# Kernel optimization log

Hardware: AMD Instinct MI355X
Metric: run time of the kernel (lower is better)

Reference implementation:

```python
import jax, jax.numpy as jnp
import numpy as np

WIDTH = 768
HEAD = 64

def setup_inputs() -> dict:
    key = jax.random.key(0)
    ks = jax.random.split(key, 8)
    x = jax.random.normal(ks[0], (8, 2048, WIDTH), dtype=jnp.float32)
    mask = jax.random.randint(ks[1], (2048, 2048), 0, 2, dtype=jnp.int32)
    s = 1.0 / np.sqrt(WIDTH)
    Wq = jax.random.normal(ks[2], (WIDTH, HEAD), dtype=jnp.float32) * s
    Wk = jax.random.normal(ks[3], (WIDTH, HEAD), dtype=jnp.float32) * s
    Wv = jax.random.normal(ks[4], (WIDTH, HEAD), dtype=jnp.float32) * s
    bq = jax.random.normal(ks[5], (HEAD,), dtype=jnp.float32) * 0.01
    bk = jax.random.normal(ks[6], (HEAD,), dtype=jnp.float32) * 0.01
    bv = jax.random.normal(ks[7], (HEAD,), dtype=jnp.float32) * 0.01
    return {"x": x, "Wq": Wq, "bq": bq, "Wk": Wk, "bk": bk, "Wv": Wv, "bv": bv, "mask": mask}

def reference(x, Wq, bq, Wk, bk, Wv, bv, mask) -> jnp.ndarray:
    # x: [B, N, width]; projections -> [B, N, head]
    Q = jnp.einsum('bnw,wh->bnh', x, Wq) + bq
    K = jnp.einsum('bnw,wh->bnh', x, Wk) + bk
    V = jnp.einsum('bnw,wh->bnh', x, Wv) + bv
    scale = 1.0 / jnp.sqrt(jnp.asarray(Q.shape[-1], dtype=Q.dtype))
    scores = jnp.einsum('bqh,bkh->bqk', Q, K) * scale  # [B, N, N]
    scores = jnp.where(mask == 0, -jnp.inf, scores)
    attn = jax.nn.softmax(scores, axis=-1)
    return jnp.einsum('bqk,bkh->bqh', attn, V)
```

## Files before the change

### kernel.cpp

```cpp
#include <hip/hip_runtime.h>

typedef short  s8v   __attribute__((ext_vector_type(8)));
typedef float  f32x4 __attribute__((ext_vector_type(4)));

#define SEQ 2048
#define WID 768

__device__ __forceinline__ unsigned fbits(float f) {
    union { float f; unsigned u; } v; v.f = f; return v.u;
}
__device__ __forceinline__ float bitsf(unsigned u) {
    union { unsigned u; float f; } v; v.u = u; return v.f;
}
__device__ __forceinline__ unsigned short f2b(float f) {
    unsigned u = fbits(f);
    return (unsigned short)((u + 0x7FFFu + ((u >> 16) & 1u)) >> 16);
}
__device__ __forceinline__ unsigned packRNE(float a, float b) {
    unsigned ta = fbits(a) + 0x7FFFu + ((fbits(a) >> 16) & 1u);
    unsigned tb = fbits(b) + 0x7FFFu + ((fbits(b) >> 16) & 1u);
    return __builtin_amdgcn_perm(tb, ta, 0x07060302u);
}
__device__ __forceinline__ unsigned packTRUNC(float a, float b) {
    return __builtin_amdgcn_perm(fbits(b), fbits(a), 0x07060302u);
}
__device__ __forceinline__ f32x4 zero4() { f32x4 z = {0.f, 0.f, 0.f, 0.f}; return z; }

__device__ __forceinline__ void async16(const unsigned short* g, unsigned short* l) {
    __builtin_amdgcn_global_load_lds(
        (const __attribute__((address_space(1))) unsigned int*)g,
        (__attribute__((address_space(3))) unsigned int*)l, 16, 0, 0);
}

__global__ __launch_bounds__(256) void convert_kernel(
    const int* __restrict__ mask,
    const float* __restrict__ Wq, const float* __restrict__ Wk, const float* __restrict__ Wv,
    unsigned short* __restrict__ WF, unsigned* __restrict__ PM)
{
    const int tid = threadIdx.x;
    const int blk = blockIdx.x;
    if (blk < 512) {
        const int gid  = blk * 4 + (tid >> 6);
        const int lane = tid & 63, quad = lane >> 4, c = lane & 15;
        const int qb = gid >> 5, kb = gid & 31;
        unsigned w = 0;
        #pragma unroll
        for (int mt = 0; mt < 2; ++mt) {
            const int q = qb * 32 + mt * 16 + c;
            #pragma unroll
            for (int i = 0; i < 4; ++i) {
                const int4 mm = *(const int4*)&mask[(size_t)q * SEQ + kb * 64 + quad * 16 + 4 * i];
                if (mm.x) w |= 1u << (mt * 16 + i * 4 + 0);
                if (mm.y) w |= 1u << (mt * 16 + i * 4 + 1);
                if (mm.z) w |= 1u << (mt * 16 + i * 4 + 2);
                if (mm.w) w |= 1u << (mt * 16 + i * 4 + 3);
            }
        }
        PM[(size_t)gid * 64 + lane] = w;
    } else {
        const int s2 = (blk - 512) * 256 + tid;
        const int chunk = s2 >> 6, l = s2 & 63;
        const int ntg = chunk / 24, r = chunk - ntg * 24;
        const int kc = r >> 1, h = r & 1;
        const int mat = ntg >> 2;
        const int col = (ntg & 3) * 16 + (l & 15);
        const int k0 = kc * 64 + h * 32 + (l >> 4) * 8;
        const float* Wm = (mat == 0) ? Wq : (mat == 1) ? Wk : Wv;
        float p[8];
        #pragma unroll
        for (int j = 0; j < 8; ++j) p[j] = Wm[(size_t)(k0 + j) * 64 + col];
        uint4 w;
        w.x = packRNE(p[0], p[1]); w.y = packRNE(p[2], p[3]);
        w.z = packRNE(p[4], p[5]); w.w = packRNE(p[6], p[7]);
        *(uint4*)&WF[(size_t)s2 * 8] = w;
    }
}

__global__ __launch_bounds__(512, 4) void qkv_proj_kernel(
    const float* __restrict__ x, const unsigned short* __restrict__ WF,
    const float* __restrict__ bq, const float* __restrict__ bk, const float* __restrict__ bv,
    unsigned short* __restrict__ QF, unsigned short* __restrict__ KF,
    unsigned short* __restrict__ VF)
{
    __shared__ unsigned short AB[2][16384];
    unsigned short (*St)[200] = (unsigned short(*)[200])AB;

    const int tid = threadIdx.x;
    const int wv = tid >> 6, lane = tid & 63, quad = lane >> 4, c = lane & 15;
    const int rg = wv >> 2, cg = wv & 3;
    const int blk = blockIdx.x;
    const int g0 = blk * 4;

    float bias[3];
    #pragma unroll
    for (int nt = 0; nt < 3; ++nt) {
        int col = cg * 48 + nt * 16 + c;
        const float* B = (col < 64) ? bq : (col < 128) ? bk : bv;
        bias[nt] = B[col & 63];
    }

    const int chunk = tid >> 6;
    const int gl = chunk >> 1, hh = chunk & 1;
    const int arow = (g0 + gl) * 16 + (lane & 15);
    const float* xrow = x + (size_t)arow * WID + hh * 32 + ((lane >> 4) & 3) * 8;

    auto issueB = [&](int kc, int b) {
        #pragma unroll
        for (int r = 0; r < 3; ++r) {
            const int e = wv * 3 + r;
            const int ntg = e >> 1, h = e & 1;
            async16(WF + (((size_t)ntg * 12 + kc) * 2 + h) * 512 + lane * 8,
                    &AB[b][4096 + (ntg * 2 + h) * 512]);
        }
    };
    auto stageA_write = [&](int b, float4 f0, float4 f1) {
        uint4 w;
        w.x = packRNE(f0.x, f0.y); w.y = packRNE(f0.z, f0.w);
        w.z = packRNE(f1.x, f1.y); w.w = packRNE(f1.z, f1.w);
        *(uint4*)&AB[b][(size_t)tid * 8] = w;
    };

    f32x4 acc[2][3];
    #pragma unroll
    for (int mt = 0; mt < 2; ++mt)
        #pragma unroll
        for (int nt = 0; nt < 3; ++nt) acc[mt][nt] = zero4();

    {
        float4 f0 = *(const float4*)&xrow[0];
        float4 f1 = *(const float4*)&xrow[4];
        stageA_write(0, f0, f1);
        issueB(0, 0);
    }

    for (int kc = 0; kc < 12; ++kc) {
        const int b = kc & 1;
        __syncthreads();
        float4 f0, f1;
        if (kc < 11) {
            f0 = *(const float4*)&xrow[(kc + 1) * 64];
            f1 = *(const float4*)&xrow[(kc + 1) * 64 + 4];
            issueB(kc + 1, b ^ 1);
        }

        s8v afr[2][2], bfr[3][2];
        #pragma unroll
        for (int mt = 0; mt < 2; ++mt)
            #pragma unroll
            for (int h = 0; h < 2; ++h)
                afr[mt][h] = *(const s8v*)&AB[b][((rg * 2 + mt) * 2 + h) * 512 + lane * 8];
        #pragma unroll
        for (int nt = 0; nt < 3; ++nt)
            #pragma unroll
            for (int h = 0; h < 2; ++h)
                bfr[nt][h] = *(const s8v*)&AB[b][4096 + ((cg * 3 + nt) * 2 + h) * 512 + lane * 8];
        #pragma unroll
        for (int h = 0; h < 2; ++h)
            #pragma unroll
            for (int mt = 0; mt < 2; ++mt)
                #pragma unroll
                for (int nt = 0; nt < 3; ++nt)
                    acc[mt][nt] = __builtin_amdgcn_mfma_f32_16x16x32_bf16(
                        afr[mt][h], bfr[nt][h], acc[mt][nt], 0, 0, 0);

        if (kc < 11) stageA_write(b ^ 1, f0, f1);
    }

    #pragma unroll
    for (int mt = 0; mt < 2; ++mt)
        #pragma unroll
        for (int nt = 0; nt < 3; ++nt)
            #pragma unroll
            for (int i = 0; i < 4; ++i)
                St[rg * 32 + mt * 16 + quad * 4 + i][cg * 48 + nt * 16 + c]
                    = f2b(acc[mt][nt][i] + bias[nt]);
    __syncthreads();

    {
        const int g = tid >> 7, ks = (tid >> 6) & 1, l = tid & 63;
        uint4 v = *(uint4*)&St[g * 16 + (l & 15)][ks * 32 + (l >> 4) * 8];
        *(uint4*)&QF[(((size_t)(g0 + g)) * 2 + ks) * 512 + (size_t)l * 8] = v;
    }
    {
        const int ksnt = tid >> 6, l = tid & 63;
        const int ks = ksnt >> 2, nt = ksnt & 3;
        uint4 v = *(uint4*)&St[4 * (l & 15) + nt][64 + ks * 32 + (l >> 4) * 8];
        *(uint4*)&KF[(((size_t)blk * 8 + ksnt) * 64 + l) * 8] = v;
    }
    {
        const int ksnt = tid >> 6, l = tid & 63;
        const int ks = ksnt >> 2, nt = ksnt & 3;
        const int d = 128 + nt * 16 + (l & 15);
        const int r0 = (l >> 4) * 16 + ks * 8;
        unsigned short p[8];
        #pragma unroll
        for (int s = 0; s < 8; ++s) p[s] = St[r0 + s][d];
        uint4 w;
        w.x = (unsigned)p[0] | ((unsigned)p[1] << 16);
        w.y = (unsigned)p[2] | ((unsigned)p[3] << 16);
        w.z = (unsigned)p[4] | ((unsigned)p[5] << 16);
        w.w = (unsigned)p[6] | ((unsigned)p[7] << 16);
        *(uint4*)&VF[(((size_t)blk * 8 + ksnt) * 64 + l) * 8] = w;
    }
}

__global__ __launch_bounds__(1024, 4) void attn_kernel(
    const unsigned short* __restrict__ QF, const unsigned short* __restrict__ KF,
    const unsigned short* __restrict__ VF, const unsigned* __restrict__ PM,
    float* __restrict__ out)
{
    __shared__ float Obuf[64][68];
    __shared__ float Lbuf[64];

    const int tid = threadIdx.x;
    const int wv = tid >> 6, lane = tid & 63, quad = lane >> 4, c = lane & 15;
    const int sl = wv & 3, qg = wv >> 2, mt = qg & 1;
    const int blk = blockIdx.x;
    const int bb = blk & 7, qt = blk >> 3;
    const size_t qrow0 = (size_t)bb * SEQ + qt * 64;

    if (tid < 64) Lbuf[tid] = 0.f;

    union Q8 { s8v v; unsigned w[4]; } qf[2];
    {
        const size_t qgrp = (size_t)bb * 128 + qt * 4 + qg;
        #pragma unroll
        for (int ks = 0; ks < 2; ++ks)
            qf[ks].v = *(const s8v*)&QF[(qgrp * 2 + ks) * 512 + (size_t)lane * 8];
    }

    f32x4 O[4];
    float lro0 = 0.f, lro1 = 0.f;
    #pragma unroll
    for (int nt = 0; nt < 4; ++nt) O[nt] = zero4();

    const unsigned* pmrow = PM + (size_t)((qt * 2 + (qg >> 1)) * 32 + sl * 8) * 64 + lane;

    #pragma unroll 1
    for (int kt = 0; kt < 8; ++kt) {
        const size_t kbg = (size_t)bb * 32 + sl * 8 + kt;
        const unsigned short* kb_ = KF + kbg * 4096 + (size_t)lane * 8;
        const unsigned short* vb_ = VF + kbg * 4096 + (size_t)lane * 8;

        const unsigned pmw = pmrow[(size_t)kt * 64];

        s8v vfr[8];
        #pragma unroll
        for (int d = 0; d < 8; ++d) vfr[d] = *(const s8v*)&vb_[(size_t)d * 512];
        s8v kfr[8];
        #pragma unroll
        for (int d = 0; d < 8; ++d) kfr[d] = *(const s8v*)&kb_[(size_t)d * 512];

        f32x4 S[4];
        #pragma unroll
        for (int nt = 0; nt < 4; ++nt) S[nt] = zero4();
        #pragma unroll
        for (int ks = 0; ks < 2; ++ks)
            #pragma unroll
            for (int nt = 0; nt < 4; ++nt)
                S[nt] = __builtin_amdgcn_mfma_f32_16x16x32_bf16(kfr[ks * 4 + nt], qf[ks].v, S[nt], 0, 0, 0);

        const unsigned pmh = pmw >> (mt * 16);
        float p[4][4];
        #pragma unroll
        for (int i = 0; i < 4; ++i)
            #pragma unroll
            for (int nt = 0; nt < 4; ++nt) {
                float e = exp2f(fmaf(S[nt][i], 0.18033688011112042f, -21.640425613334451f));
                p[nt][i] = ((pmh >> (i * 4 + nt)) & 1u) ? e : 0.f;
            }
        union { unsigned w[8]; s8v v[2]; } P;
        #pragma unroll
        for (int j = 0; j < 8; ++j) {
            unsigned uu = packTRUNC(p[2 * (j & 1)][j >> 1], p[2 * (j & 1) + 1][j >> 1]);
            P.w[j] = uu;
            if (j & 1) lro1 += bitsf(uu << 16) + bitsf(uu & 0xFFFF0000u);
            else       lro0 += bitsf(uu << 16) + bitsf(uu & 0xFFFF0000u);
        }

        #pragma unroll
        for (int ks = 0; ks < 2; ++ks)
            #pragma unroll
            for (int nt = 0; nt < 4; ++nt)
                O[nt] = __builtin_amdgcn_mfma_f32_16x16x32_bf16(P.v[ks], vfr[ks * 4 + nt], O[nt], 0, 0, 0);
    }

    #pragma unroll
    for (int j = 0; j < 5; ++j) {
        int idx = tid + 1024 * j;
        if (idx < 64 * 68) ((float*)Obuf)[idx] = 0.f;
    }
    __syncthreads();

    {
        float l = lro0 + lro1;
        l += __shfl_xor(l, 16);
        l += __shfl_xor(l, 32);
        if (quad == 0) atomicAdd(&Lbuf[qg * 16 + c], l);
    }
    #pragma unroll
    for (int i = 0; i < 4; ++i)
        #pragma unroll
        for (int nt = 0; nt < 4; ++nt)
            atomicAdd(&Obuf[qg * 16 + quad * 4 + i][nt * 16 + c], O[nt][i]);
    __syncthreads();
    {
        const int r = tid >> 4, d4 = (tid & 15) * 4;
        const float invL = 1.0f / Lbuf[r];
        float4 v = *(float4*)&Obuf[r][d4];
        float4 o = make_float4(v.x * invL, v.y * invL, v.z * invL, v.w * invL);
        *(float4*)&out[(qrow0 + r) * 64 + d4] = o;
    }
}

extern "C" void kernel_launch(void* const* d_in, const int* in_sizes, int n_in,
                              void* d_out, int out_size, void* d_ws, size_t ws_size,
                              hipStream_t stream)
{
    const float* x    = (const float*)d_in[0];
    const float* Wq   = (const float*)d_in[1];
    const float* bq   = (const float*)d_in[2];
    const float* Wk   = (const float*)d_in[3];
    const float* bk   = (const float*)d_in[4];
    const float* Wv   = (const float*)d_in[5];
    const float* bv   = (const float*)d_in[6];
    const int*   mask = (const int*)d_in[7];
    float* out = (float*)d_out;

    unsigned short* QF = (unsigned short*)d_ws;
    unsigned short* KF = QF + (size_t)16384 * 64;
    unsigned short* VF = KF + (size_t)16384 * 64;
    unsigned short* WF = VF + (size_t)16384 * 64;
    unsigned*       PM = (unsigned*)(WF + (size_t)192 * WID);

    convert_kernel<<<584, 256, 0, stream>>>(mask, Wq, Wk, Wv, WF, PM);
    qkv_proj_kernel<<<256, 512, 0, stream>>>(x, WF, bq, bk, bv, QF, KF, VF);
    attn_kernel<<<256, 1024, 0, stream>>>(QF, KF, VF, PM, out);
}
```

Measured before the change: 159.6 us.

## Fuse QKV projection and attention into one kernel with per-batch grid barrier

Merges the QKV projection and attention kernels into a single 1024-thread kernel. A global atomic counter per batch, reset by a memset before launch, lets each block wait until the 32 blocks that produce its batch's K/V have finished before it starts attention. The projection is re-tiled so 1024 threads each handle a single m-tile. This removes a kernel launch and the gap between kernels, and lets attention for one batch start while other batches are still projecting. In exchange it relies on all 256 blocks being co-resident to avoid deadlock, adds spin-wait overhead, and lowers the occupancy bound to 2 blocks.

```diff
diff --git a/kernel.cpp b/kernel.cpp
--- a/kernel.cpp
+++ b/kernel.cpp
@@ -76,240 +76,242 @@
     }
 }
 
-__global__ __launch_bounds__(512, 4) void qkv_proj_kernel(
+__global__ __launch_bounds__(1024, 2) void fused_pa(
     const float* __restrict__ x, const unsigned short* __restrict__ WF,
     const float* __restrict__ bq, const float* __restrict__ bk, const float* __restrict__ bv,
+    const unsigned* __restrict__ PM,
     unsigned short* __restrict__ QF, unsigned short* __restrict__ KF,
-    unsigned short* __restrict__ VF)
+    unsigned short* __restrict__ VF, float* __restrict__ out,
+    unsigned* __restrict__ bar)
 {
-    __shared__ unsigned short AB[2][16384];
-    unsigned short (*St)[200] = (unsigned short(*)[200])AB;
+    __shared__ __align__(16) unsigned char SMEM[65536];
 
     const int tid = threadIdx.x;
     const int wv = tid >> 6, lane = tid & 63, quad = lane >> 4, c = lane & 15;
-    const int rg = wv >> 2, cg = wv & 3;
     const int blk = blockIdx.x;
-    const int g0 = blk * 4;
-
-    float bias[3];
-    #pragma unroll
-    for (int nt = 0; nt < 3; ++nt) {
-        int col = cg * 48 + nt * 16 + c;
-        const float* B = (col < 64) ? bq : (col < 128) ? bk : bv;
-        bias[nt] = B[col & 63];
+
+    {
+        unsigned short (*AB)[16384] = (unsigned short(*)[16384])SMEM;
+        unsigned short (*St)[200]   = (unsigned short(*)[200])SMEM;
+        const int g0 = blk * 4;
+        const int rg = wv >> 2, cg = wv & 3;
+
+        float bias[3];
+        #pragma unroll
+        for (int nt = 0; nt < 3; ++nt) {
+            int col = cg * 48 + nt * 16 + c;
+            const float* B = (col < 64) ? bq : (col < 128) ? bk : bv;
+            bias[nt] = B[col & 63];
+        }
+
+        const int ach = tid >> 7;
+        const int agl = ach >> 1, ah = ach & 1;
+        const int al  = (tid >> 1) & 63;
+        const int aj0 = (tid & 1) * 4;
+        const float* xptr = x + (size_t)((g0 + agl) * 16 + (al & 15)) * WID
+                              + ah * 32 + (al >> 4) * 8 + aj0;
+
+        auto issueB = [&](int kc, int b) {
+            if (wv < 12) {
+                #pragma unroll
+                for (int r = 0; r < 2; ++r) {
+                    const int e = wv * 2 + r;
+                    const int ntg = e >> 1, h = e & 1;
+                    async16(WF + (((size_t)ntg * 12 + kc) * 2 + h) * 512 + lane * 8,
+                            &AB[b][4096 + (ntg * 2 + h) * 512]);
+                }
+            }
+        };
+        auto stageA = [&](int b, float4 f) {
+            uint2 w2;
+            w2.x = packRNE(f.x, f.y);
+            w2.y = packRNE(f.z, f.w);
+            *(uint2*)&AB[b][(size_t)tid * 4] = w2;
+        };
+
+        f32x4 acc[3];
+        #pragma unroll
+        for (int nt = 0; nt < 3; ++nt) acc[nt] = zero4();
+
+        {
+            float4 f = *(const float4*)&xptr[0];
+            stageA(0, f);
+            issueB(0, 0);
+        }
+
+        for (int kc = 0; kc < 12; ++kc) {
+            const int b = kc & 1;
+            __syncthreads();
+            float4 f;
+            if (kc < 11) {
+                f = *(const float4*)&xptr[(kc + 1) * 64];
+                issueB(kc + 1, b ^ 1);
+            }
+
+            s8v afr[2], bfr[3][2];
+            #pragma unroll
+            for (int h = 0; h < 2; ++h)
+                afr[h] = *(const s8v*)&AB[b][(rg * 2 + h) * 512 + lane * 8];
+            #pragma unroll
+            for (int nt = 0; nt < 3; ++nt)
+                #pragma unroll
+                for (int h = 0; h < 2; ++h)
+                    bfr[nt][h] = *(const s8v*)&AB[b][4096 + ((cg * 3 + nt) * 2 + h) * 512 + lane * 8];
+            #pragma unroll
+            for (int h = 0; h < 2; ++h)
+                #pragma unroll
+                for (int nt = 0; nt < 3; ++nt)
+                    acc[nt] = __builtin_amdgcn_mfma_f32_16x16x32_bf16(
+                        afr[h], bfr[nt][h], acc[nt], 0, 0, 0);
+
+            if (kc < 11) stageA(b ^ 1, f);
+        }
+
+        #pragma unroll
+        for (int nt = 0; nt < 3; ++nt)
+            #pragma unroll
+            for (int i = 0; i < 4; ++i)
+                St[rg * 16 + quad * 4 + i][cg * 48 + nt * 16 + c]
+                    = f2b(acc[nt][i] + bias[nt]);
+        __syncthreads();
+
+        if (tid < 512) {
+            const int g = tid >> 7, ks = (tid >> 6) & 1, l = tid & 63;
+            uint4 v = *(uint4*)&St[g * 16 + (l & 15)][ks * 32 + (l >> 4) * 8];
+            *(uint4*)&QF[(((size_t)(g0 + g)) * 2 + ks) * 512 + (size_t)l * 8] = v;
+        } else {
+            const int t2 = tid - 512;
+            const int ksnt = t2 >> 6, l = t2 & 63;
+            const int ks = ksnt >> 2, nt = ksnt & 3;
+            uint4 v = *(uint4*)&St[4 * (l & 15) + nt][64 + ks * 32 + (l >> 4) * 8];
+            *(uint4*)&KF[(((size_t)blk * 8 + ksnt) * 64 + l) * 8] = v;
+        }
+        if (tid < 512) {
+            const int ksnt = tid >> 6, l = tid & 63;
+            const int ks = ksnt >> 2, nt = ksnt & 3;
+            const int d = 128 + nt * 16 + (l & 15);
+            const int r0 = (l >> 4) * 16 + ks * 8;
+            unsigned short p[8];
+            #pragma unroll
+            for (int s = 0; s < 8; ++s) p[s] = St[r0 + s][d];
+            uint4 w;
+            w.x = (unsigned)p[0] | ((unsigned)p[1] << 16);
+            w.y = (unsigned)p[2] | ((unsigned)p[3] << 16);
+            w.z = (unsigned)p[4] | ((unsigned)p[5] << 16);
+            w.w = (unsigned)p[6] | ((unsigned)p[7] << 16);
+            *(uint4*)&VF[(((size_t)blk * 8 + ksnt) * 64 + l) * 8] = w;
+        }
     }
 
-    const int chunk = tid >> 6;
-    const int gl = chunk >> 1, hh = chunk & 1;
-    const int arow = (g0 + gl) * 16 + (lane & 15);
-    const float* xrow = x + (size_t)arow * WID + hh * 32 + ((lane >> 4) & 3) * 8;
-
-    auto issueB = [&](int kc, int b) {
-        #pragma unroll
-        for (int r = 0; r < 3; ++r) {
-            const int e = wv * 3 + r;
-            const int ntg = e >> 1, h = e & 1;
-            async16(WF + (((size_t)ntg * 12 + kc) * 2 + h) * 512 + lane * 8,
-                    &AB[b][4096 + (ntg * 2 + h) * 512]);
-        }
-    };
-    auto stageA_write = [&](int b, float4 f0, float4 f1) {
-        uint4 w;
-        w.x = packRNE(f0.x, f0.y); w.y = packRNE(f0.z, f0.w);
-        w.z = packRNE(f1.x, f1.y); w.w = packRNE(f1.z, f1.w);
-        *(uint4*)&AB[b][(size_t)tid * 8] = w;
-    };
-
-    f32x4 acc[2][3];
-    #pragma unroll
-    for (int mt = 0; mt < 2; ++mt)
-        #pragma unroll
-        for (int nt = 0; nt < 3; ++nt) acc[mt][nt] = zero4();
-
-    {
-        float4 f0 = *(const float4*)&xrow[0];
-        float4 f1 = *(const float4*)&xrow[4];
-        stageA_write(0, f0, f1);
-        issueB(0, 0);
-    }
-
-    for (int kc = 0; kc < 12; ++kc) {
-        const int b = kc & 1;
-        __syncthreads();
-        float4 f0, f1;
-        if (kc < 11) {
-            f0 = *(const float4*)&xrow[(kc + 1) * 64];
-            f1 = *(const float4*)&xrow[(kc + 1) * 64 + 4];
-            issueB(kc + 1, b ^ 1);
-        }
-
-        s8v afr[2][2], bfr[3][2];
-        #pragma unroll
-        for (int mt = 0; mt < 2; ++mt)
-            #pragma unroll
-            for (int h = 0; h < 2; ++h)
-                afr[mt][h] = *(const s8v*)&AB[b][((rg * 2 + mt) * 2 + h) * 512 + lane * 8];
-        #pragma unroll
-        for (int nt = 0; nt < 3; ++nt)
-            #pragma unroll
-            for (int h = 0; h < 2; ++h)
-                bfr[nt][h] = *(const s8v*)&AB[b][4096 + ((cg * 3 + nt) * 2 + h) * 512 + lane * 8];
-        #pragma unroll
-        for (int h = 0; h < 2; ++h)
-            #pragma unroll
-            for (int mt = 0; mt < 2; ++mt)
-                #pragma unroll
-                for (int nt = 0; nt < 3; ++nt)
-                    acc[mt][nt] = __builtin_amdgcn_mfma_f32_16x16x32_bf16(
-                        afr[mt][h], bfr[nt][h], acc[mt][nt], 0, 0, 0);
-
-        if (kc < 11) stageA_write(b ^ 1, f0, f1);
-    }
-
-    #pragma unroll
-    for (int mt = 0; mt < 2; ++mt)
-        #pragma unroll
-        for (int nt = 0; nt < 3; ++nt)
-            #pragma unroll
-            for (int i = 0; i < 4; ++i)
-                St[rg * 32 + mt * 16 + quad * 4 + i][cg * 48 + nt * 16 + c]
-                    = f2b(acc[mt][nt][i] + bias[nt]);
     __syncthreads();
-
-    {
-        const int g = tid >> 7, ks = (tid >> 6) & 1, l = tid & 63;
-        uint4 v = *(uint4*)&St[g * 16 + (l & 15)][ks * 32 + (l >> 4) * 8];
-        *(uint4*)&QF[(((size_t)(g0 + g)) * 2 + ks) * 512 + (size_t)l * 8] = v;
-    }
-    {
-        const int ksnt = tid >> 6, l = tid & 63;
-        const int ks = ksnt >> 2, nt = ksnt & 3;
-        uint4 v = *(uint4*)&St[4 * (l & 15) + nt][64 + ks * 32 + (l >> 4) * 8];
-        *(uint4*)&KF[(((size_t)blk * 8 + ksnt) * 64 + l) * 8] = v;
-    }
-    {
-        const int ksnt = tid >> 6, l = tid & 63;
-        const int ks = ksnt >> 2, nt = ksnt & 3;
-        const int d = 128 + nt * 16 + (l & 15);
-        const int r0 = (l >> 4) * 16 + ks * 8;
-        unsigned short p[8];
-        #pragma unroll
-        for (int s = 0; s < 8; ++s) p[s] = St[r0 + s][d];
-        uint4 w;
-        w.x = (unsigned)p[0] | ((unsigned)p[1] << 16);
-        w.y = (unsigned)p[2] | ((unsigned)p[3] << 16);
-        w.z = (unsigned)p[4] | ((unsigned)p[5] << 16);
-        w.w = (unsigned)p[6] | ((unsigned)p[7] << 16);
-        *(uint4*)&VF[(((size_t)blk * 8 + ksnt) * 64 + l) * 8] = w;
-    }
-}
-
-__global__ __launch_bounds__(1024, 4) void attn_kernel(
-    const unsigned short* __restrict__ QF, const unsigned short* __restrict__ KF,
-    const unsigned short* __restrict__ VF, const unsigned* __restrict__ PM,
-    float* __restrict__ out)
-{
-    __shared__ float Obuf[64][68];
-    __shared__ float Lbuf[64];
-
-    const int tid = threadIdx.x;
-    const int wv = tid >> 6, lane = tid & 63, quad = lane >> 4, c = lane & 15;
-    const int sl = wv & 3, qg = wv >> 2, mt = qg & 1;
-    const int blk = blockIdx.x;
-    const int bb = blk & 7, qt = blk >> 3;
-    const size_t qrow0 = (size_t)bb * SEQ + qt * 64;
-
-    if (tid < 64) Lbuf[tid] = 0.f;
-
-    union Q8 { s8v v; unsigned w[4]; } qf[2];
-    {
-        const size_t qgrp = (size_t)bb * 128 + qt * 4 + qg;
-        #pragma unroll
-        for (int ks = 0; ks < 2; ++ks)
-            qf[ks].v = *(const s8v*)&QF[(qgrp * 2 + ks) * 512 + (size_t)lane * 8];
-    }
-
-    f32x4 O[4];
-    float lro0 = 0.f, lro1 = 0.f;
-    #pragma unroll
-    for (int nt = 0; nt < 4; ++nt) O[nt] = zero4();
-
-    const unsigned* pmrow = PM + (size_t)((qt * 2 + (qg >> 1)) * 32 + sl * 8) * 64 + lane;
-
-    #pragma unroll 1
-    for (int kt = 0; kt < 8; ++kt) {
-        const size_t kbg = (size_t)bb * 32 + sl * 8 + kt;
-        const unsigned short* kb_ = KF + kbg * 4096 + (size_t)lane * 8;
-        const unsigned short* vb_ = VF + kbg * 4096 + (size_t)lane * 8;
-
-        const unsigned pmw = pmrow[(size_t)kt * 64];
-
-        s8v vfr[8];
-        #pragma unroll
-        for (int d = 0; d < 8; ++d) vfr[d] = *(const s8v*)&vb_[(size_t)d * 512];
-        s8v kfr[8];
-        #pragma unroll
-        for (int d = 0; d < 8; ++d) kfr[d] = *(const s8v*)&kb_[(size_t)d * 512];
-
-        f32x4 S[4];
-        #pragma unroll
-        for (int nt = 0; nt < 4; ++nt) S[nt] = zero4();
-        #pragma unroll
-        for (int ks = 0; ks < 2; ++ks)
-            #pragma unroll
-            for (int nt = 0; nt < 4; ++nt)
-                S[nt] = __builtin_amdgcn_mfma_f32_16x16x32_bf16(kfr[ks * 4 + nt], qf[ks].v, S[nt], 0, 0, 0);
-
-        const unsigned pmh = pmw >> (mt * 16);
-        float p[4][4];
-        #pragma unroll
-        for (int i = 0; i < 4; ++i)
-            #pragma unroll
-            for (int nt = 0; nt < 4; ++nt) {
-                float e = exp2f(fmaf(S[nt][i], 0.18033688011112042f, -21.640425613334451f));
-                p[nt][i] = ((pmh >> (i * 4 + nt)) & 1u) ? e : 0.f;
-            }
-        union { unsigned w[8]; s8v v[2]; } P;
-        #pragma unroll
-        for (int j = 0; j < 8; ++j) {
-            unsigned uu = packTRUNC(p[2 * (j & 1)][j >> 1], p[2 * (j & 1) + 1][j >> 1]);
-            P.w[j] = uu;
-            if (j & 1) lro1 += bitsf(uu << 16) + bitsf(uu & 0xFFFF0000u);
-            else       lro0 += bitsf(uu << 16) + bitsf(uu & 0xFFFF0000u);
-        }
-
-        #pragma unroll
-        for (int ks = 0; ks < 2; ++ks)
-            #pragma unroll
-            for (int nt = 0; nt < 4; ++nt)
-                O[nt] = __builtin_amdgcn_mfma_f32_16x16x32_bf16(P.v[ks], vfr[ks * 4 + nt], O[nt], 0, 0, 0);
-    }
-
-    #pragma unroll
-    for (int j = 0; j < 5; ++j) {
-        int idx = tid + 1024 * j;
-        if (idx < 64 * 68) ((float*)Obuf)[idx] = 0.f;
+    if (tid == 0) {
+        __threadfence();
+        atomicAdd(&bar[blk >> 5], 1u);
+        while (atomicAdd(&bar[blk & 7], 0u) < 32u)
+            __builtin_amdgcn_s_sleep(2);
     }
     __syncthreads();
 
     {
-        float l = lro0 + lro1;
-        l += __shfl_xor(l, 16);
-        l += __shfl_xor(l, 32);
-        if (quad == 0) atomicAdd(&Lbuf[qg * 16 + c], l);
-    }
-    #pragma unroll
-    for (int i = 0; i < 4; ++i)
-        #pragma unroll
-        for (int nt = 0; nt < 4; ++nt)
-            atomicAdd(&Obuf[qg * 16 + quad * 4 + i][nt * 16 + c], O[nt][i]);
-    __syncthreads();
-    {
-        const int r = tid >> 4, d4 = (tid & 15) * 4;
-        const float invL = 1.0f / Lbuf[r];
-        float4 v = *(float4*)&Obuf[r][d4];
-        float4 o = make_float4(v.x * invL, v.y * invL, v.z * invL, v.w * invL);
-        *(float4*)&out[(qrow0 + r) * 64 + d4] = o;
+        float (*Obuf)[68] = (float(*)[68])SMEM;
+        float* Lbuf       = (float*)(SMEM + 17408);
+
+        const int sl = wv & 3, qg = wv >> 2, mt = qg & 1;
+        const int bb = blk & 7, qt = blk >> 3;
+        const size_t qrow0 = (size_t)bb * SEQ + qt * 64;
+
+        if (tid < 64) Lbuf[tid] = 0.f;
+
+        union Q8 { s8v v; unsigned w[4]; } qf[2];
+        {
+            const size_t qgrp = (size_t)bb * 128 + qt * 4 + qg;
+            #pragma unroll
+            for (int ks = 0; ks < 2; ++ks)
+                qf[ks].v = *(const s8v*)&QF[(qgrp * 2 + ks) * 512 + (size_t)lane * 8];
+        }
+
+        f32x4 O[4];
+        float lro0 = 0.f, lro1 = 0.f;
+        #pragma unroll
+        for (int nt = 0; nt < 4; ++nt) O[nt] = zero4();
+
+        const unsigned* pmrow = PM + (size_t)((qt * 2 + (qg >> 1)) * 32 + sl * 8) * 64 + lane;
+
+        #pragma unroll 1
+        for (int kt = 0; kt < 8; ++kt) {
+            const size_t kbg = (size_t)bb * 32 + sl * 8 + kt;
+            const unsigned short* kb_ = KF + kbg * 4096 + (size_t)lane * 8;
+            const unsigned short* vb_ = VF + kbg * 4096 + (size_t)lane * 8;
+
+            const unsigned pmw = pmrow[(size_t)kt * 64];
+
+            s8v vfr[8];
+            #pragma unroll
+            for (int d = 0; d < 8; ++d) vfr[d] = *(const s8v*)&vb_[(size_t)d * 512];
+            s8v kfr[8];
+            #pragma unroll
+            for (int d = 0; d < 8; ++d) kfr[d] = *(const s8v*)&kb_[(size_t)d * 512];
+
+            f32x4 S[4];
+            #pragma unroll
+            for (int nt = 0; nt < 4; ++nt) S[nt] = zero4();
+            #pragma unroll
+            for (int ks = 0; ks < 2; ++ks)
+                #pragma unroll
+                for (int nt = 0; nt < 4; ++nt)
+                    S[nt] = __builtin_amdgcn_mfma_f32_16x16x32_bf16(kfr[ks * 4 + nt], qf[ks].v, S[nt], 0, 0, 0);
+
+            const unsigned pmh = pmw >> (mt * 16);
+            float p[4][4];
+            #pragma unroll
+            for (int i = 0; i < 4; ++i)
+                #pragma unroll
+                for (int nt = 0; nt < 4; ++nt) {
+                    float e = exp2f(fmaf(S[nt][i], 0.18033688011112042f, -21.640425613334451f));
+                    p[nt][i] = ((pmh >> (i * 4 + nt)) & 1u) ? e : 0.f;
+                }
+            union { unsigned w[8]; s8v v[2]; } P;
+            #pragma unroll
+            for (int j = 0; j < 8; ++j) {
+                unsigned uu = packTRUNC(p[2 * (j & 1)][j >> 1], p[2 * (j & 1) + 1][j >> 1]);
+                P.w[j] = uu;
+                if (j & 1) lro1 += bitsf(uu << 16) + bitsf(uu & 0xFFFF0000u);
+                else       lro0 += bitsf(uu << 16) + bitsf(uu & 0xFFFF0000u);
+            }
+
+            #pragma unroll
+            for (int ks = 0; ks < 2; ++ks)
+                #pragma unroll
+                for (int nt = 0; nt < 4; ++nt)
+                    O[nt] = __builtin_amdgcn_mfma_f32_16x16x32_bf16(P.v[ks], vfr[ks * 4 + nt], O[nt], 0, 0, 0);
+        }
+
+        #pragma unroll
+        for (int j = 0; j < 5; ++j) {
+            int idx = tid + 1024 * j;
+            if (idx < 64 * 68) ((float*)Obuf)[idx] = 0.f;
+        }
+        __syncthreads();
+
+        {
+            float l = lro0 + lro1;
+            l += __shfl_xor(l, 16);
+            l += __shfl_xor(l, 32);
+            if (quad == 0) atomicAdd(&Lbuf[qg * 16 + c], l);
+        }
+        #pragma unroll
+        for (int i = 0; i < 4; ++i)
+            #pragma unroll
+            for (int nt = 0; nt < 4; ++nt)
+                atomicAdd(&Obuf[qg * 16 + quad * 4 + i][nt * 16 + c], O[nt][i]);
+        __syncthreads();
+        {
+            const int r = tid >> 4, d4 = (tid & 15) * 4;
+            const float invL = 1.0f / Lbuf[r];
+            float4 v = *(float4*)&Obuf[r][d4];
+            float4 o = make_float4(v.x * invL, v.y * invL, v.z * invL, v.w * invL);
+            *(float4*)&out[(qrow0 + r) * 64 + d4] = o;
+        }
     }
 }
 
@@ -332,8 +334,9 @@
     unsigned short* VF = KF + (size_t)16384 * 64;
     unsigned short* WF = VF + (size_t)16384 * 64;
     unsigned*       PM = (unsigned*)(WF + (size_t)192 * WID);
-
+    unsigned*       bar = PM + (size_t)2048 * 64;
+
+    hipMemsetAsync(bar, 0, 32, stream);
     convert_kernel<<<584, 256, 0, stream>>>(mask, Wq, Wk, Wv, WF, PM);
-    qkv_proj_kernel<<<256, 512, 0, stream>>>(x, WF, bq, bk, bv, QF, KF, VF);
-    attn_kernel<<<256, 1024, 0, stream>>>(QF, KF, VF, PM, out);
-}
+    fused_pa<<<256, 1024, 0, stream>>>(x, WF, bq, bk, bv, PM, QF, KF, VF, out, bar);
+}
```

Measured after the change: 172.1 us. 1.08x slower.
